# Kernel tuning notes

Hardware: AMD Instinct MI355X
Metric: run time of the kernel (lower is better)

## Reference

```python
import jax, jax.numpy as jnp
import numpy as np

G = 8  # order of C8 rotation group

def expand_circulant(w):
    # w: [out_fields, in_fields, G] free params of a C8 regular->regular 1x1 conv.
    # Full weight: W[of*G+go, if*G+gi] = w[of, if, (go-gi) mod G]
    g = jnp.arange(G)
    idx = (g[:, None] - g[None, :]) % G            # [go, gi]
    Wf = w[:, :, idx]                              # [of, if, go, gi]
    Wf = jnp.transpose(Wf, (0, 2, 1, 3))           # [of, go, if, gi]
    return Wf.reshape(w.shape[0] * G, w.shape[1] * G)

def eq_proj(x2, w, b):
    # x2: [B, in_fields*G]; equivariant 1x1 conv = GEMM with circulant-expanded weight
    Wf = expand_circulant(w)                       # [out_fields*G, in_fields*G]
    bf = jnp.repeat(b, G)                          # per-field bias, shared across group dim
    return x2 @ Wf.T + bf

def setup_inputs() -> dict:
    key = jax.random.key(0)
    ks = jax.random.split(key, 12)
    B, d_model, n_head, d_k, d_v = 8192, 128, 8, 64, 64
    C = d_model * G                                # 1024
    s_in = 0.02
    inp = {
        'q': jax.random.normal(ks[0], (B, C, 1, 1), jnp.float32),
        'k': jax.random.normal(ks[1], (B, C, 1, 1), jnp.float32),
        'v': jax.random.normal(ks[2], (B, C, 1, 1), jnp.float32),
        'w_q': jax.random.normal(ks[3], (n_head * d_k, d_model, G), jnp.float32) * s_in,
        'b_q': jnp.zeros((n_head * d_k,), jnp.float32),
        'w_k': jax.random.normal(ks[4], (n_head * d_k, d_model, G), jnp.float32) * s_in,
        'b_k': jnp.zeros((n_head * d_k,), jnp.float32),
        'w_v': jax.random.normal(ks[5], (n_head * d_v, d_model, G), jnp.float32) * s_in,
        'b_v': jnp.zeros((n_head * d_v,), jnp.float32),
        'w_fc': jax.random.normal(ks[6], (d_model, n_head * d_v, G), jnp.float32) * s_in,
        'b_fc': jnp.zeros((d_model,), jnp.float32),
    }
    return inp

def reference(q, k, v, w_q, b_q, w_k, b_k, w_v, b_v, w_fc, b_fc):
    B, C = q.shape[0], q.shape[1]
    n_head, d_k = 8, 64
    d_v = 64
    temp = jnp.asarray(d_k ** 0.5, q.dtype)
    residual = q                                   # [B, C, 1, 1]
    q2 = q.reshape(B, C)
    k2 = k.reshape(B, C)
    v2 = v.reshape(B, C)
    # equivariant 1x1 conv projections -> [B, n_head*d_k*G]
    qp = eq_proj(q2, w_q, b_q).reshape(B, G, n_head, d_k).transpose(0, 2, 1, 3)  # [B,H,G,dk]
    kp = eq_proj(k2, w_k, b_k).reshape(B, G, n_head, d_k).transpose(0, 2, 1, 3)
    vp = eq_proj(v2, w_v, b_v).reshape(B, G, n_head, d_v).transpose(0, 2, 1, 3)
    # scaled dot-product attention over the G=8 group/orientation positions
    attn = jax.nn.softmax(jnp.einsum('bhqd,bhkd->bhqk', qp / temp, kp), axis=-1)  # [B,H,G,G]
    out = jnp.einsum('bhqk,bhkd->bhqd', attn, vp)  # [B,H,G,dv]
    # transpose(1,2) then flatten, exactly as torch .view(sz_b, -1, 1, 1)
    out = out.transpose(0, 2, 1, 3).reshape(B, G * n_head * d_v)
    out = eq_proj(out, w_fc, b_fc)                 # [B, d_model*G]
    out = out.reshape(B, C, 1, 1) + residual
    return out, attn
```

## Files before the change

### kernel.cpp

```cpp
#include <hip/hip_runtime.h>
#include <hip/hip_bf16.h>

typedef unsigned short u16;
typedef unsigned int u32;
typedef __bf16 bf16x8_t __attribute__((ext_vector_type(8)));
typedef float f32x4_t __attribute__((ext_vector_type(4)));

__device__ __forceinline__ float b2f(u16 v) {
  return __uint_as_float(((u32)v) << 16);
}
__device__ __forceinline__ u16 f2b(float f) {
  __hip_bfloat16 h = __float2bfloat16(f);
  return *reinterpret_cast<u16*>(&h);
}
__device__ __forceinline__ float blo(u32 u) { return __uint_as_float(u << 16); }
__device__ __forceinline__ float bhi(u32 u) { return __uint_as_float(u & 0xffff0000u); }

__device__ __forceinline__ void async_lds16(const u16* g, u16* l) {
  __builtin_amdgcn_global_load_lds(
      (__attribute__((address_space(1))) void*)g,
      (__attribute__((address_space(3))) void*)l, 16, 0, 0);
}

__device__ __forceinline__ void expand8(const float* __restrict__ w,
                                        u16* __restrict__ dst, int I,
                                        int kshift, int gid) {
  const int n = gid >> kshift;
  const int kc = (gid & ((1 << kshift) - 1)) * 8;
  const int K = 8 << kshift;
  const float* wp = w + (size_t)((n >> 3) * I + (kc >> 3)) * 8;
  float4 w0 = *(const float4*)wp;
  float4 w1 = *(const float4*)(wp + 4);
  float w8[8] = {w0.x, w0.y, w0.z, w0.w, w1.x, w1.y, w1.z, w1.w};
  u16 t[8];
  const int r = (n - kc) & 7;
#pragma unroll
  for (int j = 0; j < 8; ++j) t[j] = f2b(w8[(r - j) & 7]);
  *(uint4*)(dst + (size_t)n * K + kc) = *(const uint4*)t;
}

__device__ __forceinline__ void cvt8(const float* __restrict__ src,
                                     u16* __restrict__ dst, int gid) {
  const float* p = src + (size_t)gid * 8;
  float4 a = *(const float4*)p;
  float4 b = *(const float4*)(p + 4);
  u16 t[8] = {f2b(a.x), f2b(a.y), f2b(a.z), f2b(a.w),
              f2b(b.x), f2b(b.y), f2b(b.z), f2b(b.w)};
  *(uint4*)(dst + (size_t)gid * 8) = *(const uint4*)t;
}

__global__ __launch_bounds__(256) void expand_all(
    const float* __restrict__ w_q, const float* __restrict__ w_k,
    const float* __restrict__ w_v, const float* __restrict__ w_fc,
    const float* __restrict__ q, const float* __restrict__ k,
    const float* __restrict__ v, u16* __restrict__ Wq, u16* __restrict__ Wk,
    u16* __restrict__ Wv, u16* __restrict__ Wfc, u16* __restrict__ qb,
    u16* __restrict__ kb, u16* __restrict__ vb, int cblocks) {
  const int e = blockIdx.x;
  if (e < 8192) {
    const int plane = e >> 11;
    const int gid = (e & 2047) * 256 + threadIdx.x;
    if (plane == 0) expand8(w_q, Wq, 128, 7, gid);
    else if (plane == 1) expand8(w_k, Wk, 128, 7, gid);
    else if (plane == 2) expand8(w_v, Wv, 128, 7, gid);
    else expand8(w_fc, Wfc, 512, 9, gid);
  } else {
    const int ce = e - 8192;
    const int plane = ce / cblocks;
    const int gid = (ce - plane * cblocks) * 256 + threadIdx.x;
    if (plane == 0) cvt8(q, qb, gid);
    else if (plane == 1) cvt8(k, kb, gid);
    else cvt8(v, vb, gid);
  }
}

__global__ __launch_bounds__(512, 2) void gemm_qkv8p(
    const u16* __restrict__ X0, const u16* __restrict__ X1,
    const u16* __restrict__ X2, const u16* __restrict__ W0,
    const u16* __restrict__ W1, const u16* __restrict__ W2,
    const float* __restrict__ b0v, const float* __restrict__ b1v,
    const float* __restrict__ b2v, u16* __restrict__ Y0, u16* __restrict__ Y1,
    u16* __restrict__ Y2, int M, int N, int K) {
  __shared__ __align__(16) u16 lds[65536];
  const int z = blockIdx.y;
  const u16* X = (z == 0) ? X0 : (z == 1) ? X1 : X2;
  const u16* W = (z == 0) ? W0 : (z == 1) ? W1 : W2;
  const float* bias = (z == 0) ? b0v : (z == 1) ? b1v : b2v;
  u16* Y = (z == 0) ? Y0 : (z == 1) ? Y1 : Y2;

  const int tid = threadIdx.x;
  const int bid = blockIdx.x;
  const int grid_m = M >> 8, grid_n = N >> 8;
  const int nb = grid_m * grid_n;
  int pid = (bid & 7) * (nb >> 3) + (bid >> 3);
  const int nig = 8 * grid_n;
  const int group_id = pid / nig;
  const int first_m = group_id * 8;
  const int gsz = min(8, grid_m - first_m);
  const int mt = first_m + (pid % gsz);
  const int ntile = (pid % nig) / gsz;
  const int m0 = mt << 8, n0 = ntile << 8;

  const int lane = tid & 63, wave = tid >> 6;
  const int wg = wave >> 2;
  const int wq = wave & 3;
  const int l16 = lane & 15, quad = lane >> 4;
  const int lswz = l16 & 7;

  const u16* gA = X + (size_t)m0 * K;
  const u16* gB = W + (size_t)n0 * K;
  const int srow = tid >> 3;
  const int skbg = (tid & 7) ^ (srow & 7);

  f32x4_t acc[8][4] = {};
  const int KT = K >> 6;
  const int niter = KT >> 1;

  auto stg = [&](int kt, int h, bool isB) {
    u16* l = lds + (isB ? 32768 : 0) + ((kt & 1) * 2 + h) * 8192 + tid * 8;
    const u16* g = (isB ? gB : gA) + (size_t)(h * 128 + srow) * K + kt * 64 +
                   skbg * 8;
    async_lds16(g, l);
    async_lds16(g + (size_t)64 * K, l + 4096);
  };
  auto ldA = [&](int kt, int mh, bf16x8_t (&a)[8]) {
    const u16* base = lds + ((kt & 1) * 2 + wg) * 8192 + (mh * 64 + l16) * 64;
#pragma unroll
    for (int mi = 0; mi < 4; ++mi)
#pragma unroll
      for (int ks = 0; ks < 2; ++ks)
        a[mi * 2 + ks] = *(const bf16x8_t*)(base + mi * 1024 +
                                            (((ks * 4 + quad) ^ lswz) * 8));
  };
  auto ldB = [&](int kt, int nh, bf16x8_t (&b)[4]) {
    const u16* base = lds + 32768 + ((kt & 1) * 2 + (wq >> 1)) * 8192 +
                      ((wq & 1) * 64 + nh * 32 + l16) * 64;
#pragma unroll
    for (int ni = 0; ni < 2; ++ni)
#pragma unroll
      for (int ks = 0; ks < 2; ++ks)
        b[ni * 2 + ks] = *(const bf16x8_t*)(base + ni * 1024 +
                                            (((ks * 4 + quad) ^ lswz) * 8));
  };
  auto mm = [&](int mh, int nh, bf16x8_t (&a)[8], bf16x8_t (&b)[4]) {
    __builtin_amdgcn_s_setprio(1);
#pragma unroll
    for (int mi = 0; mi < 4; ++mi)
#pragma unroll
      for (int ni = 0; ni < 2; ++ni)
#pragma unroll
        for (int ks = 0; ks < 2; ++ks)
          acc[mh * 4 + mi][nh * 2 + ni] = __builtin_amdgcn_mfma_f32_16x16x32_bf16(
              a[mi * 2 + ks], b[ni * 2 + ks], acc[mh * 4 + mi][nh * 2 + ni], 0,
              0, 0);
    __builtin_amdgcn_s_setprio(0);
  };
  auto bar = [] { __builtin_amdgcn_s_barrier(); };
  auto lgkm0 = [] {
    asm volatile("s_waitcnt lgkmcnt(0)" ::: "memory");
    __builtin_amdgcn_sched_barrier(0);
  };
  auto sched = [] { __builtin_amdgcn_sched_barrier(0); };

  bf16x8_t a0[8], a1[8], b0[4], b1[4];

  stg(0, 0, false); sched();
  stg(0, 0, true);  sched();
  stg(0, 1, false); sched();
  stg(0, 1, true);  sched();
  stg(1, 0, true);  sched();
  stg(1, 0, false); sched();
  asm volatile("s_waitcnt vmcnt(4)" ::: "memory");
  bar();
  sched();

  for (int it = 0; it < niter; ++it) {
    const int t = it * 2;
    const bool more = (t + 2 < KT);
    ldA(t, 0, a0); ldB(t, 0, b0);
    stg(t + 1, 1, false);
    sched(); bar(); lgkm0();
    mm(0, 0, a0, b0);
    bar();
    ldB(t, 1, b1);
    stg(t + 1, 1, true);
    sched(); bar(); lgkm0();
    mm(0, 1, a0, b1);
    bar();
    ldA(t, 1, a1);
    if (more) stg(t + 2, 0, true);
    sched(); bar(); lgkm0();
    mm(1, 1, a1, b1);
    bar();
    if (more) stg(t + 2, 0, false);
    sched();
    if (more) asm volatile("s_waitcnt vmcnt(4)" ::: "memory");
    else      asm volatile("s_waitcnt vmcnt(0)" ::: "memory");
    bar(); lgkm0();
    mm(1, 0, a1, b0);
    bar();
    ldA(t + 1, 0, a0); ldB(t + 1, 0, b0);
    if (more) stg(t + 2, 1, false);
    sched(); bar(); lgkm0();
    mm(0, 0, a0, b0);
    bar();
    ldB(t + 1, 1, b1);
    if (more) stg(t + 2, 1, true);
    sched(); bar(); lgkm0();
    mm(0, 1, a0, b1);
    bar();
    ldA(t + 1, 1, a1);
    if (more) stg(t + 3, 0, true);
    sched(); bar(); lgkm0();
    mm(1, 1, a1, b1);
    bar();
    if (more) {
      stg(t + 3, 0, false);
      sched();
      asm volatile("s_waitcnt vmcnt(4)" ::: "memory");
      bar(); lgkm0();
      mm(1, 0, a1, b0);
      bar();
    } else {
      lgkm0();
      mm(1, 0, a1, b0);
    }
  }

#pragma unroll
  for (int ni = 0; ni < 4; ++ni) {
    const int col = n0 + wq * 64 + ni * 16 + l16;
    const float bv = bias[col >> 3];
#pragma unroll
    for (int mi = 0; mi < 8; ++mi) {
#pragma unroll
      for (int r = 0; r < 4; ++r) {
        const int rw = m0 + wg * 128 + mi * 16 + quad * 4 + r;
        Y[(size_t)rw * N + col] = f2b(acc[mi][ni][r] + bv);
      }
    }
  }
}

template <int TM, int TN, bool HAS_RES, bool OUT_F32>
__device__ __forceinline__ void gemm_pipe(
    const u16* __restrict__ X, const u16* __restrict__ W,
    const float* __restrict__ bias, const float* __restrict__ res,
    void* __restrict__ Yv, int M, int N, int K, int bid) {
  constexpr int LDS_A = TM * 32;
  constexpr int BUF = (TM + TN) * 32;
  constexpr int APASS = TM / 128, BPASS = TN / 128;
  constexpr int LPT = APASS + BPASS;
  constexpr int NJ = TN / 64;
  constexpr int FH = TM / 64;
  __shared__ __align__(16) u16 lds[4 * BUF];

  const int tid = threadIdx.x;
  const int grid_m = M / TM, grid_n = N / TN;
  const int nb = grid_m * grid_n;
  int pid = (bid & 7) * (nb >> 3) + (bid >> 3);
  const int nig = 8 * grid_n;
  const int group_id = pid / nig;
  const int first_m = group_id * 8;
  const int gsz = min(8, grid_m - first_m);
  const int mt = first_m + (pid % gsz);
  const int ntile = (pid % nig) / gsz;
  const int m0 = mt * TM, n0 = ntile * TN;

  const int lane = tid & 63, wave = tid >> 6;
  const int wm = (wave >> 2) * (TM / 2);
  const int wn = (wave & 3) * (TN / 4);
  const int l16 = lane & 15, quad = lane >> 4;
  const int kbl = quad ^ ((l16 >> 1) & 3);

  const int srow = tid >> 2;
  const int skbg = (tid & 3) ^ ((tid >> 3) & 3);
  const u16* pA = X + (size_t)(m0 + srow) * K + skbg * 8;
  const u16* pB = W + (size_t)(n0 + srow) * K + skbg * 8;
  const size_t rskip = (size_t)128 * K;

  const int aoff = (wm + l16) * 32 + kbl * 8;
  const int boff = LDS_A + (wn + l16) * 32 + kbl * 8;

  f32x4_t acc[2 * FH][NJ] = {};
  const int nt = K >> 5;

  auto stage = [&](int t) {
    u16* l = lds + (t & 3) * BUF;
    const u16* a = pA + t * 32;
    const u16* b = pB + t * 32;
#pragma unroll
    for (int p = 0; p < APASS; ++p)
      async_lds16(a + p * rskip, l + tid * 8 + p * 4096);
#pragma unroll
    for (int p = 0; p < BPASS; ++p)
      async_lds16(b + p * rskip, l + LDS_A + tid * 8 + p * 4096);
  };

#define WAIT_VM_LPT()                                              \
  do {                                                             \
    if constexpr (LPT == 4)                                        \
      asm volatile("s_waitcnt vmcnt(4)" ::: "memory");             \
    else if constexpr (LPT == 3)                                   \
      asm volatile("s_waitcnt vmcnt(3)" ::: "memory");             \
    else                                                           \
      asm volatile("s_waitcnt vmcnt(2)" ::: "memory");             \
  } while (0)

  bf16x8_t A0[FH], A1[FH], Bc[NJ], Bn[NJ];

  stage(0);
  __builtin_amdgcn_sched_barrier(0);
  stage(1);
  __builtin_amdgcn_sched_barrier(0);
  stage(2);
  WAIT_VM_LPT();
  __builtin_amdgcn_s_barrier();
  __builtin_amdgcn_sched_barrier(0);

  {
    const u16* la = lds + aoff;
    const u16* lb = lds + boff;
#pragma unroll
    for (int mi = 0; mi < FH; ++mi) A0[mi] = *(const bf16x8_t*)(la + mi * 512);
#pragma unroll
    for (int ni = 0; ni < NJ; ++ni) Bc[ni] = *(const bf16x8_t*)(lb + ni * 512);
  }

  auto body = [&](int t, bf16x8_t (&BCUR)[NJ], bf16x8_t (&BNXT)[NJ]) {
    if (t + 3 < nt) stage(t + 3);
    const u16* lc = lds + (t & 3) * BUF;
    const u16* ln = lds + ((t + 1) & 3) * BUF;
#pragma unroll
    for (int mi = 0; mi < FH; ++mi)
      A1[mi] = *(const bf16x8_t*)(lc + aoff + (mi + FH) * 512);
    if (t + 1 < nt) {
#pragma unroll
      for (int ni = 0; ni < NJ; ++ni)
        BNXT[ni] = *(const bf16x8_t*)(ln + boff + ni * 512);
    }
    __builtin_amdgcn_s_setprio(1);
#pragma unroll
    for (int mi = 0; mi < FH; ++mi)
#pragma unroll
      for (int ni = 0; ni < NJ; ++ni)
        acc[mi][ni] = __builtin_amdgcn_mfma_f32_16x16x32_bf16(
            A0[mi], BCUR[ni], acc[mi][ni], 0, 0, 0);
    __builtin_amdgcn_s_setprio(0);
    if (t + 1 < nt) {
#pragma unroll
      for (int mi = 0; mi < FH; ++mi)
        A0[mi] = *(const bf16x8_t*)(ln + aoff + mi * 512);
    }
    __builtin_amdgcn_s_setprio(1);
#pragma unroll
    for (int mi = 0; mi < FH; ++mi)
#pragma unroll
      for (int ni = 0; ni < NJ; ++ni)
        acc[mi + FH][ni] = __builtin_amdgcn_mfma_f32_16x16x32_bf16(
            A1[mi], BCUR[ni], acc[mi + FH][ni], 0, 0, 0);
    __builtin_amdgcn_s_setprio(0);
    if (t + 1 < nt) {
      asm volatile("s_waitcnt lgkmcnt(0)" ::: "memory");
      __builtin_amdgcn_sched_barrier(0);
      if (t + 3 < nt) WAIT_VM_LPT();
      else            asm volatile("s_waitcnt vmcnt(0)" ::: "memory");
      __builtin_amdgcn_s_barrier();
      __builtin_amdgcn_sched_barrier(0);
    }
  };

  for (int t = 0; t < nt; t += 2) {
    body(t, Bc, Bn);
    body(t + 1, Bn, Bc);
  }
#undef WAIT_VM_LPT

#pragma unroll
  for (int ni = 0; ni < NJ; ++ni) {
    const int col = n0 + wn + ni * 16 + l16;
    const float bv = bias[col >> 3];
#pragma unroll
    for (int mi = 0; mi < 2 * FH; ++mi) {
#pragma unroll
      for (int r = 0; r < 4; ++r) {
        const int rw = m0 + wm + mi * 16 + quad * 4 + r;
        float vv = acc[mi][ni][r] + bv;
        if (HAS_RES) vv += res[(size_t)rw * N + col];
        if (OUT_F32)
          ((float*)Yv)[(size_t)rw * N + col] = vv;
        else
          ((u16*)Yv)[(size_t)rw * N + col] = f2b(vv);
      }
    }
  }
}

__global__ __launch_bounds__(512, 2) void gemm_fc(
    const u16* __restrict__ X, const u16* __restrict__ W,
    const float* __restrict__ bias, const float* __restrict__ res,
    float* __restrict__ Y, int M, int N, int K) {
  gemm_pipe<128, 128, true, true>(X, W, bias, res, Y, M, N, K, blockIdx.x);
}

__global__ __launch_bounds__(256) void attn_kernel(
    const u16* __restrict__ qp, const u16* __restrict__ kp,
    const u16* __restrict__ vp, float* __restrict__ probs,
    u16* __restrict__ o, int iters) {
  __shared__ __align__(16) u16 Qs[4][8 * 72];
  __shared__ __align__(16) u16 Ks[4][8 * 72];
  __shared__ __align__(16) float Ps[4][64];
  const int tid = threadIdx.x;
  const int wave = tid >> 6;
  const int lane = tid & 63;
  const int r = lane >> 3, c = lane & 7;
  const int ls = r * 72 + c * 8;
  const int qg = r;
  const int kg = c;

  auto pairof = [&](int it) { return (it * gridDim.x + blockIdx.x) * 4 + wave; };
  auto gaddr = [&](int it) {
    const int pr = pairof(it);
    return (size_t)(pr >> 3) * 4096 + (size_t)r * 512 + (pr & 7) * 64 + c * 8;
  };

  uint4 qr = *(const uint4*)(qp + gaddr(0));
  uint4 kr = *(const uint4*)(kp + gaddr(0));

  for (int it = 0; it < iters; ++it) {
    *(uint4*)&Qs[wave][ls] = qr;
    *(uint4*)&Ks[wave][ls] = kr;
    const int pair = pairof(it);
    const int b = pair >> 3;
    const int h = pair & 7;
    float vcf[8];
#pragma unroll
    for (int k2 = 0; k2 < 8; ++k2)
      vcf[k2] = b2f(vp[(size_t)b * 4096 + (size_t)k2 * 512 + h * 64 + lane]);
    if (it + 1 < iters) {
      qr = *(const uint4*)(qp + gaddr(it + 1));
      kr = *(const uint4*)(kp + gaddr(it + 1));
    }
    float s = 0.f;
#pragma unroll
    for (int d8 = 0; d8 < 8; ++d8) {
      uint4 qa = *(const uint4*)&Qs[wave][qg * 72 + d8 * 8];
      uint4 ka = *(const uint4*)&Ks[wave][kg * 72 + d8 * 8];
      s += blo(qa.x) * blo(ka.x) + bhi(qa.x) * bhi(ka.x);
      s += blo(qa.y) * blo(ka.y) + bhi(qa.y) * bhi(ka.y);
      s += blo(qa.z) * blo(ka.z) + bhi(qa.z) * bhi(ka.z);
      s += blo(qa.w) * blo(ka.w) + bhi(qa.w) * bhi(ka.w);
    }
    s *= 0.125f;
    float mx = s;
    mx = fmaxf(mx, __shfl_xor(mx, 1));
    mx = fmaxf(mx, __shfl_xor(mx, 2));
    mx = fmaxf(mx, __shfl_xor(mx, 4));
    float e = __expf(s - mx);
    float sum = e;
    sum += __shfl_xor(sum, 1);
    sum += __shfl_xor(sum, 2);
    sum += __shfl_xor(sum, 4);
    const float p = e / sum;
    probs[(size_t)pair * 64 + lane] = p;
    Ps[wave][lane] = p;
#pragma unroll
    for (int q2 = 0; q2 < 8; ++q2) {
      float4 p0 = *(const float4*)&Ps[wave][q2 * 8];
      float4 p1 = *(const float4*)&Ps[wave][q2 * 8 + 4];
      float acc = p0.x * vcf[0] + p0.y * vcf[1] + p0.z * vcf[2] + p0.w * vcf[3] +
                  p1.x * vcf[4] + p1.y * vcf[5] + p1.z * vcf[6] + p1.w * vcf[7];
      o[(size_t)b * 4096 + q2 * 512 + h * 64 + lane] = f2b(acc);
    }
  }
}

extern "C" void kernel_launch(void* const* d_in, const int* in_sizes, int n_in,
                              void* d_out, int out_size, void* d_ws, size_t ws_size,
                              hipStream_t stream) {
  const float* q = (const float*)d_in[0];
  const float* k = (const float*)d_in[1];
  const float* v = (const float*)d_in[2];
  const float* w_q = (const float*)d_in[3];
  const float* b_q = (const float*)d_in[4];
  const float* w_k = (const float*)d_in[5];
  const float* b_k = (const float*)d_in[6];
  const float* w_v = (const float*)d_in[7];
  const float* b_v = (const float*)d_in[8];
  const float* w_fc = (const float*)d_in[9];
  const float* b_fc = (const float*)d_in[10];

  const int B = in_sizes[0] / 1024;
  float* out = (float*)d_out;
  float* probs = out + (size_t)B * 1024;

  u16* Wq = (u16*)d_ws;
  u16* Wk = Wq + (size_t)4096 * 1024;
  u16* Wv = Wk + (size_t)4096 * 1024;
  u16* Wfc = Wv + (size_t)4096 * 1024;
  u16* qb = Wfc + (size_t)4096 * 1024;
  u16* kb = qb + (size_t)B * 1024;
  u16* vb = kb + (size_t)B * 1024;
  u16* scratch = vb + (size_t)B * 1024;
  const size_t fixed_bytes =
      ((size_t)4 * 4096 * 1024 + (size_t)3 * B * 1024) * sizeof(u16);

  const size_t per_row = (size_t)(4 * 4096) * sizeof(u16);
  int chunkB = 256;
  for (int c = B; c >= 256; c >>= 1) {
    if (fixed_bytes + (size_t)c * per_row <= ws_size) { chunkB = c; break; }
  }

  u16* qp = scratch;
  u16* kp = qp + (size_t)chunkB * 4096;
  u16* vp = kp + (size_t)chunkB * 4096;
  u16* ao = vp + (size_t)chunkB * 4096;

  const int cblocks = B / 2;
  expand_all<<<8192 + 3 * cblocks, 256, 0, stream>>>(
      w_q, w_k, w_v, w_fc, q, k, v, Wq, Wk, Wv, Wfc, qb, kb, vb, cblocks);

  for (int cs = 0; cs < B; cs += chunkB) {
    const int nb_p = (chunkB / 256) * (4096 / 256);
    gemm_qkv8p<<<dim3(nb_p, 3), 512, 0, stream>>>(
        qb + (size_t)cs * 1024, kb + (size_t)cs * 1024, vb + (size_t)cs * 1024,
        Wq, Wk, Wv, b_q, b_k, b_v, qp, kp, vp, chunkB, 4096, 1024);
    const int ablocks = (chunkB >= 1024) ? 2048 : chunkB * 2;
    const int aiters = (chunkB * 8) / (ablocks * 4);
    attn_kernel<<<ablocks, 256, 0, stream>>>(qp, kp, vp,
                                             probs + (size_t)cs * 512, ao, aiters);
    const int nb_fc = (chunkB / 128) * (1024 / 128);
    gemm_fc<<<nb_fc, 512, 0, stream>>>(ao, Wfc, b_fc, q + (size_t)cs * 1024,
                                       out + (size_t)cs * 1024, chunkB, 1024,
                                       4096);
  }
}
```

Baseline: 578.9 us.

## Replace pipelined FC GEMM with simple BK=64 kernel and alias attention output

Swaps the 4-stage async-LDS pipelined 512-thread FC GEMM for a simpler 256-thread kernel that loads BK=64 tiles with XOR swizzle and syncs twice per k-step. It also writes the attention output in place over the q-projection buffer, which shrinks per-row workspace so larger chunks can fit. A 64-wide N-tile variant is used when chunks are small. The loss of load/compute overlap in the FC GEMM may cost throughput, and the aliasing means attention must finish reading q before its output overwrites it. Restrict was dropped on the affected pointers to reflect the aliasing.

```diff
diff --git a/kernel.cpp b/kernel.cpp
--- a/kernel.cpp
+++ b/kernel.cpp
@@ -5,6 +5,8 @@
 typedef unsigned int u32;
 typedef __bf16 bf16x8_t __attribute__((ext_vector_type(8)));
 typedef float f32x4_t __attribute__((ext_vector_type(4)));
+
+#define BK 64
 
 __device__ __forceinline__ float b2f(u16 v) {
   return __uint_as_float(((u32)v) << 16);
@@ -242,21 +244,16 @@
   }
 }
 
-template <int TM, int TN, bool HAS_RES, bool OUT_F32>
-__device__ __forceinline__ void gemm_pipe(
-    const u16* __restrict__ X, const u16* __restrict__ W,
+template <int TN, bool HAS_RES, bool OUT_F32>
+__device__ __forceinline__ void gemm_core(
+    const u16* __restrict__ Xb, const u16* __restrict__ W,
     const float* __restrict__ bias, const float* __restrict__ res,
     void* __restrict__ Yv, int M, int N, int K, int bid) {
-  constexpr int LDS_A = TM * 32;
-  constexpr int BUF = (TM + TN) * 32;
-  constexpr int APASS = TM / 128, BPASS = TN / 128;
-  constexpr int LPT = APASS + BPASS;
-  constexpr int NJ = TN / 64;
-  constexpr int FH = TM / 64;
-  __shared__ __align__(16) u16 lds[4 * BUF];
-
+  __shared__ __align__(16) u16 As[128 * BK];
+  __shared__ __align__(16) u16 Bs[TN * BK];
   const int tid = threadIdx.x;
-  const int grid_m = M / TM, grid_n = N / TN;
+
+  const int grid_m = M >> 7, grid_n = N / TN;
   const int nb = grid_m * grid_n;
   int pid = (bid & 7) * (nb >> 3) + (bid >> 3);
   const int nig = 8 * grid_n;
@@ -264,128 +261,63 @@
   const int first_m = group_id * 8;
   const int gsz = min(8, grid_m - first_m);
   const int mt = first_m + (pid % gsz);
-  const int ntile = (pid % nig) / gsz;
-  const int m0 = mt * TM, n0 = ntile * TN;
-
-  const int lane = tid & 63, wave = tid >> 6;
-  const int wm = (wave >> 2) * (TM / 2);
-  const int wn = (wave & 3) * (TN / 4);
-  const int l16 = lane & 15, quad = lane >> 4;
-  const int kbl = quad ^ ((l16 >> 1) & 3);
-
-  const int srow = tid >> 2;
-  const int skbg = (tid & 3) ^ ((tid >> 3) & 3);
-  const u16* pA = X + (size_t)(m0 + srow) * K + skbg * 8;
-  const u16* pB = W + (size_t)(n0 + srow) * K + skbg * 8;
-  const size_t rskip = (size_t)128 * K;
-
-  const int aoff = (wm + l16) * 32 + kbl * 8;
-  const int boff = LDS_A + (wn + l16) * 32 + kbl * 8;
-
-  f32x4_t acc[2 * FH][NJ] = {};
-  const int nt = K >> 5;
-
-  auto stage = [&](int t) {
-    u16* l = lds + (t & 3) * BUF;
-    const u16* a = pA + t * 32;
-    const u16* b = pB + t * 32;
-#pragma unroll
-    for (int p = 0; p < APASS; ++p)
-      async_lds16(a + p * rskip, l + tid * 8 + p * 4096);
-#pragma unroll
-    for (int p = 0; p < BPASS; ++p)
-      async_lds16(b + p * rskip, l + LDS_A + tid * 8 + p * 4096);
-  };
-
-#define WAIT_VM_LPT()                                              \
-  do {                                                             \
-    if constexpr (LPT == 4)                                        \
-      asm volatile("s_waitcnt vmcnt(4)" ::: "memory");             \
-    else if constexpr (LPT == 3)                                   \
-      asm volatile("s_waitcnt vmcnt(3)" ::: "memory");             \
-    else                                                           \
-      asm volatile("s_waitcnt vmcnt(2)" ::: "memory");             \
-  } while (0)
-
-  bf16x8_t A0[FH], A1[FH], Bc[NJ], Bn[NJ];
-
-  stage(0);
-  __builtin_amdgcn_sched_barrier(0);
-  stage(1);
-  __builtin_amdgcn_sched_barrier(0);
-  stage(2);
-  WAIT_VM_LPT();
-  __builtin_amdgcn_s_barrier();
-  __builtin_amdgcn_sched_barrier(0);
-
-  {
-    const u16* la = lds + aoff;
-    const u16* lb = lds + boff;
-#pragma unroll
-    for (int mi = 0; mi < FH; ++mi) A0[mi] = *(const bf16x8_t*)(la + mi * 512);
-#pragma unroll
-    for (int ni = 0; ni < NJ; ++ni) Bc[ni] = *(const bf16x8_t*)(lb + ni * 512);
-  }
-
-  auto body = [&](int t, bf16x8_t (&BCUR)[NJ], bf16x8_t (&BNXT)[NJ]) {
-    if (t + 3 < nt) stage(t + 3);
-    const u16* lc = lds + (t & 3) * BUF;
-    const u16* ln = lds + ((t + 1) & 3) * BUF;
-#pragma unroll
-    for (int mi = 0; mi < FH; ++mi)
-      A1[mi] = *(const bf16x8_t*)(lc + aoff + (mi + FH) * 512);
-    if (t + 1 < nt) {
-#pragma unroll
-      for (int ni = 0; ni < NJ; ++ni)
-        BNXT[ni] = *(const bf16x8_t*)(ln + boff + ni * 512);
-    }
-    __builtin_amdgcn_s_setprio(1);
-#pragma unroll
-    for (int mi = 0; mi < FH; ++mi)
-#pragma unroll
-      for (int ni = 0; ni < NJ; ++ni)
-        acc[mi][ni] = __builtin_amdgcn_mfma_f32_16x16x32_bf16(
-            A0[mi], BCUR[ni], acc[mi][ni], 0, 0, 0);
-    __builtin_amdgcn_s_setprio(0);
-    if (t + 1 < nt) {
-#pragma unroll
-      for (int mi = 0; mi < FH; ++mi)
-        A0[mi] = *(const bf16x8_t*)(ln + aoff + mi * 512);
-    }
-    __builtin_amdgcn_s_setprio(1);
-#pragma unroll
-    for (int mi = 0; mi < FH; ++mi)
-#pragma unroll
-      for (int ni = 0; ni < NJ; ++ni)
-        acc[mi + FH][ni] = __builtin_amdgcn_mfma_f32_16x16x32_bf16(
-            A1[mi], BCUR[ni], acc[mi + FH][ni], 0, 0, 0);
-    __builtin_amdgcn_s_setprio(0);
-    if (t + 1 < nt) {
-      asm volatile("s_waitcnt lgkmcnt(0)" ::: "memory");
-      __builtin_amdgcn_sched_barrier(0);
-      if (t + 3 < nt) WAIT_VM_LPT();
-      else            asm volatile("s_waitcnt vmcnt(0)" ::: "memory");
-      __builtin_amdgcn_s_barrier();
-      __builtin_amdgcn_sched_barrier(0);
-    }
-  };
-
-  for (int t = 0; t < nt; t += 2) {
-    body(t, Bc, Bn);
-    body(t + 1, Bn, Bc);
-  }
-#undef WAIT_VM_LPT
-
-#pragma unroll
-  for (int ni = 0; ni < NJ; ++ni) {
-    const int col = n0 + wn + ni * 16 + l16;
+  const int nt = (pid % nig) / gsz;
+  const int m0 = mt << 7, n0 = nt * TN;
+
+  const int lane = tid & 63;
+  const int wave = tid >> 6;
+  const int wm = (wave >> 1) * 64;
+  const int wn = (wave & 1) * (TN / 2);
+  const int l16 = lane & 15;
+  const int quad = lane >> 4;
+  constexpr int NJ = TN >> 5;
+
+  f32x4_t acc[4][NJ] = {};
+
+  const int row0 = tid >> 3;
+  const int kgl = ((tid & 7) ^ (row0 & 7)) * 8;
+
+  for (int k0 = 0; k0 < K; k0 += BK) {
+#pragma unroll
+    for (int it = 0; it < TN / 32; ++it)
+      async_lds16(W + (size_t)(n0 + row0 + it * 32) * K + (k0 + kgl),
+                  &Bs[(tid + it * 256) * 8]);
+#pragma unroll
+    for (int it = 0; it < 4; ++it)
+      async_lds16(Xb + (size_t)(m0 + row0 + it * 32) * K + (k0 + kgl),
+                  &As[(tid + it * 256) * 8]);
+    __syncthreads();
+#pragma unroll
+    for (int half = 0; half < 2; ++half) {
+      bf16x8_t af[4], bfr[NJ];
+#pragma unroll
+      for (int i = 0; i < 4; ++i)
+        af[i] = *(const bf16x8_t*)&As[(wm + i * 16 + l16) * BK +
+                                      (((quad + half * 4) ^ (l16 & 7)) * 8)];
+#pragma unroll
+      for (int j = 0; j < NJ; ++j)
+        bfr[j] = *(const bf16x8_t*)&Bs[(wn + j * 16 + l16) * BK +
+                                       (((quad + half * 4) ^ (l16 & 7)) * 8)];
+#pragma unroll
+      for (int i = 0; i < 4; ++i)
+#pragma unroll
+        for (int j = 0; j < NJ; ++j)
+          acc[i][j] =
+              __builtin_amdgcn_mfma_f32_16x16x32_bf16(af[i], bfr[j], acc[i][j], 0, 0, 0);
+    }
+    __syncthreads();
+  }
+
+#pragma unroll
+  for (int j = 0; j < NJ; ++j) {
+    const int col = n0 + wn + j * 16 + l16;
     const float bv = bias[col >> 3];
 #pragma unroll
-    for (int mi = 0; mi < 2 * FH; ++mi) {
+    for (int i = 0; i < 4; ++i) {
 #pragma unroll
       for (int r = 0; r < 4; ++r) {
-        const int rw = m0 + wm + mi * 16 + quad * 4 + r;
-        float vv = acc[mi][ni][r] + bv;
+        const int rw = m0 + wm + i * 16 + quad * 4 + r;
+        float vv = acc[i][j][r] + bv;
         if (HAS_RES) vv += res[(size_t)rw * N + col];
         if (OUT_F32)
           ((float*)Yv)[(size_t)rw * N + col] = vv;
@@ -396,17 +328,23 @@
   }
 }
 
-__global__ __launch_bounds__(512, 2) void gemm_fc(
+__global__ __launch_bounds__(256) void gemm_fc128(
     const u16* __restrict__ X, const u16* __restrict__ W,
     const float* __restrict__ bias, const float* __restrict__ res,
     float* __restrict__ Y, int M, int N, int K) {
-  gemm_pipe<128, 128, true, true>(X, W, bias, res, Y, M, N, K, blockIdx.x);
+  gemm_core<128, true, true>(X, W, bias, res, Y, M, N, K, blockIdx.x);
+}
+__global__ __launch_bounds__(256) void gemm_fc64(
+    const u16* __restrict__ X, const u16* __restrict__ W,
+    const float* __restrict__ bias, const float* __restrict__ res,
+    float* __restrict__ Y, int M, int N, int K) {
+  gemm_core<64, true, true>(X, W, bias, res, Y, M, N, K, blockIdx.x);
 }
 
 __global__ __launch_bounds__(256) void attn_kernel(
-    const u16* __restrict__ qp, const u16* __restrict__ kp,
+    const u16* qp, const u16* __restrict__ kp,
     const u16* __restrict__ vp, float* __restrict__ probs,
-    u16* __restrict__ o, int iters) {
+    u16* o, int iters) {
   __shared__ __align__(16) u16 Qs[4][8 * 72];
   __shared__ __align__(16) u16 Ks[4][8 * 72];
   __shared__ __align__(16) float Ps[4][64];
@@ -505,7 +443,7 @@
   const size_t fixed_bytes =
       ((size_t)4 * 4096 * 1024 + (size_t)3 * B * 1024) * sizeof(u16);
 
-  const size_t per_row = (size_t)(4 * 4096) * sizeof(u16);
+  const size_t per_row = (size_t)(3 * 4096) * sizeof(u16);
   int chunkB = 256;
   for (int c = B; c >= 256; c >>= 1) {
     if (fixed_bytes + (size_t)c * per_row <= ws_size) { chunkB = c; break; }
@@ -514,7 +452,7 @@
   u16* qp = scratch;
   u16* kp = qp + (size_t)chunkB * 4096;
   u16* vp = kp + (size_t)chunkB * 4096;
-  u16* ao = vp + (size_t)chunkB * 4096;
+  u16* ao = qp;
 
   const int cblocks = B / 2;
   expand_all<<<8192 + 3 * cblocks, 256, 0, stream>>>(
@@ -529,9 +467,18 @@
     const int aiters = (chunkB * 8) / (ablocks * 4);
     attn_kernel<<<ablocks, 256, 0, stream>>>(qp, kp, vp,
                                              probs + (size_t)cs * 512, ao, aiters);
-    const int nb_fc = (chunkB / 128) * (1024 / 128);
-    gemm_fc<<<nb_fc, 512, 0, stream>>>(ao, Wfc, b_fc, q + (size_t)cs * 1024,
-                                       out + (size_t)cs * 1024, chunkB, 1024,
-                                       4096);
-  }
-}
+    if (chunkB >= 8192) {
+      const int nb_fc = (chunkB / 128) * (1024 / 128);
+      gemm_fc128<<<nb_fc, 256, 0, stream>>>(ao, Wfc, b_fc,
+                                            q + (size_t)cs * 1024,
+                                            out + (size_t)cs * 1024, chunkB,
+                                            1024, 4096);
+    } else {
+      const int nb_fc = (chunkB / 128) * (1024 / 64);
+      gemm_fc64<<<nb_fc, 256, 0, stream>>>(ao, Wfc, b_fc,
+                                           q + (size_t)cs * 1024,
+                                           out + (size_t)cs * 1024, chunkB,
+                                           1024, 4096);
+    }
+  }
+}
```

New measurement: 601.8 us. 4.0% more time.
